# Performance work log

Measured on AMD Instinct MI355X. Metric: run time of the kernel, lower is better.

Reference implementation:

```python
import jax, jax.numpy as jnp
import numpy as np

N0, N1, N2 = 200000, 50000, 12500
E0, E1, E2 = 3200000, 800000, 200000
CIN, C, COUT = 4, 128, 1


def gcn(x, W, b, src, dst, n):
    # GCN conv with added self-loops and symmetric degree normalization
    h = x @ W
    loops = jnp.arange(n)
    s = jnp.concatenate([src, loops])
    d = jnp.concatenate([dst, loops])
    deg = jax.ops.segment_sum(jnp.ones(s.shape[0], h.dtype), d, num_segments=n)
    inv = jax.lax.rsqrt(jnp.maximum(deg, 1.0))
    msg = h[s] * (inv[s] * inv[d])[:, None]
    return jax.ops.segment_sum(msg, d, num_segments=n) + b


def pool_max(x, clusters, n_clusters):
    # cluster-based max pooling; empty clusters -> 0
    p = jax.ops.segment_max(x, clusters, num_segments=n_clusters)
    return jnp.where(jnp.isneginf(p), jnp.zeros_like(p), p)


def setup_inputs() -> dict:
    ks = jax.random.split(jax.random.key(0), 40)

    def w(k, i, o):
        return jax.random.normal(k, (i, o), jnp.float32) / np.float32(np.sqrt(i))

    inp = {
        'x': jax.random.normal(ks[0], (N0, CIN), jnp.float32),
        'edge_index0': jax.random.randint(ks[1], (2, E0), 0, N0),
        'edge_index1': jax.random.randint(ks[2], (2, E1), 0, N1),
        'edge_index2': jax.random.randint(ks[3], (2, E2), 0, N2),
        'clusters0': jax.random.randint(ks[4], (N0,), 0, N1),
        'clusters1': jax.random.randint(ks[5], (N1,), 0, N2),
        # encoder level 0
        'w_e0a': w(ks[6], CIN, C), 'b_e0a': jnp.zeros((C,), jnp.float32),
        'w_e0b': w(ks[7], C, C),   'b_e0b': jnp.zeros((C,), jnp.float32),
        # encoder level 1
        'w_e1a': w(ks[8], C, C),   'b_e1a': jnp.zeros((C,), jnp.float32),
        'w_e1b': w(ks[9], C, C),   'b_e1b': jnp.zeros((C,), jnp.float32),
        # bottom level 2
        'w_ba': w(ks[10], C, C),   'b_ba': jnp.zeros((C,), jnp.float32),
        'w_bb': w(ks[11], C, C),   'b_bb': jnp.zeros((C,), jnp.float32),
        # decoder level 1 (concat skip -> 2C in)
        'w_d1a': w(ks[12], 2 * C, C), 'b_d1a': jnp.zeros((C,), jnp.float32),
        'w_d1b': w(ks[13], C, C),     'b_d1b': jnp.zeros((C,), jnp.float32),
        # decoder level 0
        'w_d0a': w(ks[14], 2 * C, C), 'b_d0a': jnp.zeros((C,), jnp.float32),
        'w_d0b': w(ks[15], C, C),     'b_d0b': jnp.zeros((C,), jnp.float32),
        # output projection
        'w_out': w(ks[16], C, COUT), 'b_out': jnp.zeros((COUT,), jnp.float32),
    }
    return inp


def reference(x, edge_index0, edge_index1, edge_index2, clusters0, clusters1,
              w_e0a, b_e0a, w_e0b, b_e0b, w_e1a, b_e1a, w_e1b, b_e1b,
              w_ba, b_ba, w_bb, b_bb, w_d1a, b_d1a, w_d1b, b_d1b,
              w_d0a, b_d0a, w_d0b, b_d0b, w_out, b_out):
    n0 = x.shape[0]
    n1 = clusters1.shape[0]
    n2 = N2
    relu = jax.nn.relu
    s0, d0 = edge_index0[0], edge_index0[1]
    s1, d1 = edge_index1[0], edge_index1[1]
    s2, d2 = edge_index2[0], edge_index2[1]

    # encoder level 0
    e0 = relu(gcn(x, w_e0a, b_e0a, s0, d0, n0))
    e0 = relu(gcn(e0, w_e0b, b_e0b, s0, d0, n0))
    # pool -> level 1
    x1 = pool_max(e0, clusters0, n1)
    e1 = relu(gcn(x1, w_e1a, b_e1a, s1, d1, n1))
    e1 = relu(gcn(e1, w_e1b, b_e1b, s1, d1, n1))
    # pool -> level 2 (bottom)
    x2 = pool_max(e1, clusters1, n2)
    bt = relu(gcn(x2, w_ba, b_ba, s2, d2, n2))
    bt = relu(gcn(bt, w_bb, b_bb, s2, d2, n2))
    # unpool -> level 1, concat skip
    u1 = jnp.concatenate([bt[clusters1], e1], axis=1)
    dl1 = relu(gcn(u1, w_d1a, b_d1a, s1, d1, n1))
    dl1 = relu(gcn(dl1, w_d1b, b_d1b, s1, d1, n1))
    # unpool -> level 0, concat skip
    u0 = jnp.concatenate([dl1[clusters0], e0], axis=1)
    dl0 = relu(gcn(u0, w_d0a, b_d0a, s0, d0, n0))
    dl0 = relu(gcn(dl0, w_d0b, b_d0b, s0, d0, n0))
    # per-node output head
    return dl0 @ w_out + b_out
```

## Files before the change

kernel.cpp:

```cpp
#include <hip/hip_runtime.h>
#include <hip/hip_fp16.h>
#include <cstdint>
#include <cstddef>

#define PN0 200000
#define PN1 50000
#define PN2 12500
#define PE0 3200000
#define PE1 800000
#define PE2 200000

#define GCAP 64
#define CCAP 32

#define P0 0
#define P1 200192
#define P2 250368
#define P3 263168
#define P4 313344
#define CNT_END 326144
#define NBUCKETS 637
#define NITEMS 4450000
#define IPB 8192
#define NBLK 544

static inline int cdiv_i(int a, int b) { return (a + b - 1) / b; }

union H4 { uint4 q; uint2 u; __half2 h[2]; };

typedef _Float16 f16x8 __attribute__((ext_vector_type(8)));
typedef float f32x4 __attribute__((ext_vector_type(4)));
union F8 { uint4 q; f16x8 f; };

__device__ inline float2 load2f(const float* p) { return *(const float2*)p; }
__device__ inline float2 load2f(const __half* p) { return __half22float2(*(const __half2*)p); }


struct BSeg {
    const int* idx[5];
    const int* src[3];
    int item_off[5];
    int P[5];
    int colb[5];
    int cap[5];
    int nN[5];
    int ioff[3];
};

__device__ inline int seg_of_item(const BSeg& s, int i) {
    int seg = 0;
#pragma unroll
    for (int t = 1; t < 5; ++t) if (i >= s.item_off[t]) seg = t;
    return seg;
}
__device__ inline int seg_of_g(const BSeg& s, int g) {
    int seg = 0;
#pragma unroll
    for (int t = 1; t < 5; ++t) if (g >= s.P[t]) seg = t;
    return seg;
}

__global__ __launch_bounds__(256) void hist_k(BSeg s, int* __restrict__ BH) {
    __shared__ int lh[640];
    int tid = threadIdx.x;
    for (int k = tid; k < 640; k += 256) lh[k] = 0;
    __syncthreads();
    int base = blockIdx.x * IPB;
#pragma unroll 4
    for (int it = 0; it < 32; ++it) {
        int i = base + it * 256 + tid;
        if (i < NITEMS) {
            int seg = seg_of_item(s, i);
            int il = i - s.item_off[seg];
            int g = s.P[seg] + s.idx[seg][il];
            atomicAdd(&lh[g >> 9], 1);
        }
    }
    __syncthreads();
    for (int k = tid; k < 640; k += 256) BH[blockIdx.x * 640 + k] = lh[k];
}

__global__ __launch_bounds__(256) void scan_bh_k(int* __restrict__ BH, int* __restrict__ BT) {
    int b = blockIdx.x;
    int tid = threadIdx.x;
    __shared__ int tsum[256];
    int v[3];
    int base = tid * 3;
    int sum = 0;
#pragma unroll
    for (int k = 0; k < 3; ++k) {
        int idx = base + k;
        v[k] = (idx < NBLK) ? BH[idx * 640 + b] : 0;
        sum += v[k];
    }
    tsum[tid] = sum;
    __syncthreads();
    for (int off = 1; off < 256; off <<= 1) {
        int t = (tid >= off) ? tsum[tid - off] : 0;
        __syncthreads();
        tsum[tid] += t;
        __syncthreads();
    }
    int excl = tsum[tid] - sum;
#pragma unroll
    for (int k = 0; k < 3; ++k) {
        int idx = base + k;
        if (idx < NBLK) { BH[idx * 640 + b] = excl; excl += v[k]; }
    }
    if (tid == 255) BT[b] = tsum[255];
}

__global__ __launch_bounds__(1024) void bb_scan_k(const int* __restrict__ BT, int* __restrict__ BB) {
    __shared__ int sm[1024];
    int tid = threadIdx.x;
    int v = (tid < NBUCKETS) ? BT[tid] : 0;
    sm[tid] = v;
    __syncthreads();
    for (int off = 1; off < 1024; off <<= 1) {
        int t = (tid >= off) ? sm[tid - off] : 0;
        __syncthreads();
        sm[tid] += t;
        __syncthreads();
    }
    if (tid < NBUCKETS) BB[tid] = sm[tid] - v;
}

__global__ __launch_bounds__(256) void scatter_k(BSeg s, const int* __restrict__ BH,
                                                 const int* __restrict__ BB, int2* __restrict__ sorted) {
    __shared__ int lr[640];
    int tid = threadIdx.x;
    for (int k = tid; k < 640; k += 256) lr[k] = 0;
    __syncthreads();
    int base = blockIdx.x * IPB;
#pragma unroll 4
    for (int it = 0; it < 32; ++it) {
        int i = base + it * 256 + tid;
        if (i < NITEMS) {
            int seg = seg_of_item(s, i);
            int il = i - s.item_off[seg];
            int g = s.P[seg] + s.idx[seg][il];
            int val = (seg < 3) ? s.src[seg][il] : il;
            int b = g >> 9;
            int r = atomicAdd(&lr[b], 1);
            int pos = BB[b] + BH[blockIdx.x * 640 + b] + r;
            sorted[pos] = make_int2(g, val);
        }
    }
}

__global__ __launch_bounds__(256) void buildc_k(BSeg s, const int2* __restrict__ sorted,
                                                const int* __restrict__ BB, const int* __restrict__ BT,
                                                int* __restrict__ col, int* __restrict__ cnt,
                                                float* __restrict__ inv) {
    int b = blockIdx.x;
    int tid = threadIdx.x;
    __shared__ int lc[512];
    for (int k = tid; k < 512; k += 256) lc[k] = 0;
    __syncthreads();
    int start = BB[b], end = start + BT[b];
    for (int i = start + tid; i < end; i += 256) {
        int2 p = sorted[i];
        int g = p.x;
        int local = g & 511;
        int slot = atomicAdd(&lc[local], 1);
        int seg = seg_of_g(s, g);
        int d = g - s.P[seg];
        int cap = s.cap[seg];
        if (slot < cap) col[s.colb[seg] + d * cap + slot] = p.y;
    }
    __syncthreads();
    for (int local = tid; local < 512; local += 256) {
        int g = (b << 9) + local;
        int seg = seg_of_g(s, g);
        int d = g - s.P[seg];
        if (d < s.nN[seg]) {
            int c = lc[local];
            cnt[g] = c;
            if (seg < 3) inv[s.ioff[seg] + d] = rsqrtf((float)(c + 1));
        }
    }
}

struct PrepW { const float* src[11]; __half* dst[11]; };
__global__ __launch_bounds__(256) void prep_w_k(PrepW p) {
    const float* w = p.src[blockIdx.x];
    __half* o = p.dst[blockIdx.x];
    for (int i = threadIdx.x; i < 16384; i += 256) {
        int k = i >> 7, n = i & 127;
        o[n * 128 + k] = __float2half(w[i]);
    }
}


__global__ __launch_bounds__(256) void agg4_k(const float* __restrict__ X, float* __restrict__ O,
                                              const int* __restrict__ deg, const int* __restrict__ col,
                                              const float* __restrict__ inv, int N) {
    int v = blockIdx.x * 256 + threadIdx.x;
    if (v >= N) return;
    float iv = inv[v];
    float4 xv = *(const float4*)(X + (size_t)v * 4);
    float ax = xv.x * iv, ay = xv.y * iv, az = xv.z * iv, aw = xv.w * iv;
    int b0 = v * GCAP, b1 = b0 + deg[v];
    for (int j = b0; j < b1; ++j) {
        int u = col[j];
        float iu = inv[u];
        float4 xu = *(const float4*)(X + (size_t)u * 4);
        ax += xu.x * iu; ay += xu.y * iu; az += xu.z * iu; aw += xu.w * iu;
    }
    float4 o; o.x = ax * iv; o.y = ay * iv; o.z = az * iv; o.w = aw * iv;
    *(float4*)(O + (size_t)v * 4) = o;
}

__global__ __launch_bounds__(256) void gemm4_k(const float* __restrict__ XA, const float* __restrict__ W,
                                               const float* __restrict__ bias, __half* __restrict__ O, int N) {
    int wid = (blockIdx.x * 256 + threadIdx.x) >> 6;
    int lane = threadIdx.x & 63;
    if (wid >= N) return;
    float4 x = *(const float4*)(XA + (size_t)wid * 4);
    int c = lane * 2;
    float2 w0 = *(const float2*)(W + c);
    float2 w1 = *(const float2*)(W + 128 + c);
    float2 w2 = *(const float2*)(W + 256 + c);
    float2 w3 = *(const float2*)(W + 384 + c);
    float2 b = *(const float2*)(bias + c);
    float ox = b.x + x.x * w0.x + x.y * w1.x + x.z * w2.x + x.w * w3.x;
    float oy = b.y + x.x * w0.y + x.y * w1.y + x.z * w2.y + x.w * w3.y;
    ox = fmaxf(ox, 0.f); oy = fmaxf(oy, 0.f);
    *(__half2*)(O + (size_t)wid * 128 + c) = __floats2half2_rn(ox, oy);
}

__global__ __launch_bounds__(256) void agg_k(const __half* __restrict__ H, __half* __restrict__ O,
                                             const int* __restrict__ deg, const int* __restrict__ col,
                                             const float* __restrict__ inv, const float* __restrict__ bias,
                                             int N) {
    int wpair = (blockIdx.x * 256 + threadIdx.x) >> 6;
    int lane = threadIdx.x & 63;
    int v = wpair * 2 + (lane >> 5);
    int l32 = lane & 31;
    if (v >= N) return;
    float iv = inv[v];
    int c4 = l32 * 4;
    float4 a0 = {0,0,0,0}, a1 = {0,0,0,0}, a2 = {0,0,0,0}, a3 = {0,0,0,0};
    int b0 = v * GCAP, b1 = b0 + deg[v];
    int j = b0;
    for (; j + 8 <= b1; j += 8) {
        int u0 = col[j],     u1 = col[j + 1], u2 = col[j + 2], u3 = col[j + 3];
        int u4 = col[j + 4], u5 = col[j + 5], u6 = col[j + 6], u7 = col[j + 7];
        H4 t0, t1, t2, t3, t4, t5, t6, t7;
        t0.u = *(const uint2*)(H + (size_t)u0 * 128 + c4);
        t1.u = *(const uint2*)(H + (size_t)u1 * 128 + c4);
        t2.u = *(const uint2*)(H + (size_t)u2 * 128 + c4);
        t3.u = *(const uint2*)(H + (size_t)u3 * 128 + c4);
        t4.u = *(const uint2*)(H + (size_t)u4 * 128 + c4);
        t5.u = *(const uint2*)(H + (size_t)u5 * 128 + c4);
        t6.u = *(const uint2*)(H + (size_t)u6 * 128 + c4);
        t7.u = *(const uint2*)(H + (size_t)u7 * 128 + c4);
        float2 p, q;
        p = __half22float2(t0.h[0]); q = __half22float2(t0.h[1]);
        a0.x += p.x; a0.y += p.y; a0.z += q.x; a0.w += q.y;
        p = __half22float2(t1.h[0]); q = __half22float2(t1.h[1]);
        a1.x += p.x; a1.y += p.y; a1.z += q.x; a1.w += q.y;
        p = __half22float2(t2.h[0]); q = __half22float2(t2.h[1]);
        a2.x += p.x; a2.y += p.y; a2.z += q.x; a2.w += q.y;
        p = __half22float2(t3.h[0]); q = __half22float2(t3.h[1]);
        a3.x += p.x; a3.y += p.y; a3.z += q.x; a3.w += q.y;
        p = __half22float2(t4.h[0]); q = __half22float2(t4.h[1]);
        a0.x += p.x; a0.y += p.y; a0.z += q.x; a0.w += q.y;
        p = __half22float2(t5.h[0]); q = __half22float2(t5.h[1]);
        a1.x += p.x; a1.y += p.y; a1.z += q.x; a1.w += q.y;
        p = __half22float2(t6.h[0]); q = __half22float2(t6.h[1]);
        a2.x += p.x; a2.y += p.y; a2.z += q.x; a2.w += q.y;
        p = __half22float2(t7.h[0]); q = __half22float2(t7.h[1]);
        a3.x += p.x; a3.y += p.y; a3.z += q.x; a3.w += q.y;
    }
    for (; j + 4 <= b1; j += 4) {
        int u0 = col[j], u1 = col[j + 1], u2 = col[j + 2], u3 = col[j + 3];
        H4 t0, t1, t2, t3;
        t0.u = *(const uint2*)(H + (size_t)u0 * 128 + c4);
        t1.u = *(const uint2*)(H + (size_t)u1 * 128 + c4);
        t2.u = *(const uint2*)(H + (size_t)u2 * 128 + c4);
        t3.u = *(const uint2*)(H + (size_t)u3 * 128 + c4);
        float2 p, q;
        p = __half22float2(t0.h[0]); q = __half22float2(t0.h[1]);
        a0.x += p.x; a0.y += p.y; a0.z += q.x; a0.w += q.y;
        p = __half22float2(t1.h[0]); q = __half22float2(t1.h[1]);
        a1.x += p.x; a1.y += p.y; a1.z += q.x; a1.w += q.y;
        p = __half22float2(t2.h[0]); q = __half22float2(t2.h[1]);
        a2.x += p.x; a2.y += p.y; a2.z += q.x; a2.w += q.y;
        p = __half22float2(t3.h[0]); q = __half22float2(t3.h[1]);
        a3.x += p.x; a3.y += p.y; a3.z += q.x; a3.w += q.y;
    }
    for (; j < b1; ++j) {
        H4 t; t.u = *(const uint2*)(H + (size_t)col[j] * 128 + c4);
        float2 p = __half22float2(t.h[0]), q = __half22float2(t.h[1]);
        a0.x += p.x; a0.y += p.y; a0.z += q.x; a0.w += q.y;
    }
    {
        H4 t; t.u = *(const uint2*)(H + (size_t)v * 128 + c4);
        float2 p = __half22float2(t.h[0]), q = __half22float2(t.h[1]);
        a1.x += p.x; a1.y += p.y; a1.z += q.x; a1.w += q.y;
    }
    float4 s;
    s.x = (a0.x + a1.x) + (a2.x + a3.x);
    s.y = (a0.y + a1.y) + (a2.y + a3.y);
    s.z = (a0.z + a1.z) + (a2.z + a3.z);
    s.w = (a0.w + a1.w) + (a2.w + a3.w);
    float4 b = *(const float4*)(bias + c4);
    H4 t;
    t.h[0] = __floats2half2_rn(fmaxf(s.x * iv + b.x, 0.f), fmaxf(s.y * iv + b.y, 0.f));
    t.h[1] = __floats2half2_rn(fmaxf(s.z * iv + b.z, 0.f), fmaxf(s.w * iv + b.w, 0.f));
    *(uint2*)(O + (size_t)v * 128 + c4) = t.u;
}

__global__ __launch_bounds__(256) void agg_head_k(const __half* __restrict__ H,
                                                  const int* __restrict__ deg, const int* __restrict__ col,
                                                  const float* __restrict__ inv, const float* __restrict__ bias,
                                                  const float* __restrict__ wout, const float* __restrict__ bout,
                                                  float* __restrict__ out, int N) {
    int wpair = (blockIdx.x * 256 + threadIdx.x) >> 6;
    int lane = threadIdx.x & 63;
    int v = wpair * 2 + (lane >> 5);
    int l32 = lane & 31;
    if (v >= N) return;
    float iv = inv[v];
    int c4 = l32 * 4;
    float4 a0 = {0,0,0,0}, a1 = {0,0,0,0}, a2 = {0,0,0,0}, a3 = {0,0,0,0};
    int b0 = v * GCAP, b1 = b0 + deg[v];
    int j = b0;
    for (; j + 8 <= b1; j += 8) {
        int u0 = col[j],     u1 = col[j + 1], u2 = col[j + 2], u3 = col[j + 3];
        int u4 = col[j + 4], u5 = col[j + 5], u6 = col[j + 6], u7 = col[j + 7];
        H4 t0, t1, t2, t3, t4, t5, t6, t7;
        t0.u = *(const uint2*)(H + (size_t)u0 * 128 + c4);
        t1.u = *(const uint2*)(H + (size_t)u1 * 128 + c4);
        t2.u = *(const uint2*)(H + (size_t)u2 * 128 + c4);
        t3.u = *(const uint2*)(H + (size_t)u3 * 128 + c4);
        t4.u = *(const uint2*)(H + (size_t)u4 * 128 + c4);
        t5.u = *(const uint2*)(H + (size_t)u5 * 128 + c4);
        t6.u = *(const uint2*)(H + (size_t)u6 * 128 + c4);
        t7.u = *(const uint2*)(H + (size_t)u7 * 128 + c4);
        float2 p, q;
        p = __half22float2(t0.h[0]); q = __half22float2(t0.h[1]);
        a0.x += p.x; a0.y += p.y; a0.z += q.x; a0.w += q.y;
        p = __half22float2(t1.h[0]); q = __half22float2(t1.h[1]);
        a1.x += p.x; a1.y += p.y; a1.z += q.x; a1.w += q.y;
        p = __half22float2(t2.h[0]); q = __half22float2(t2.h[1]);
        a2.x += p.x; a2.y += p.y; a2.z += q.x; a2.w += q.y;
        p = __half22float2(t3.h[0]); q = __half22float2(t3.h[1]);
        a3.x += p.x; a3.y += p.y; a3.z += q.x; a3.w += q.y;
        p = __half22float2(t4.h[0]); q = __half22float2(t4.h[1]);
        a0.x += p.x; a0.y += p.y; a0.z += q.x; a0.w += q.y;
        p = __half22float2(t5.h[0]); q = __half22float2(t5.h[1]);
        a1.x += p.x; a1.y += p.y; a1.z += q.x; a1.w += q.y;
        p = __half22float2(t6.h[0]); q = __half22float2(t6.h[1]);
        a2.x += p.x; a2.y += p.y; a2.z += q.x; a2.w += q.y;
        p = __half22float2(t7.h[0]); q = __half22float2(t7.h[1]);
        a3.x += p.x; a3.y += p.y; a3.z += q.x; a3.w += q.y;
    }
    for (; j + 4 <= b1; j += 4) {
        int u0 = col[j], u1 = col[j + 1], u2 = col[j + 2], u3 = col[j + 3];
        H4 t0, t1, t2, t3;
        t0.u = *(const uint2*)(H + (size_t)u0 * 128 + c4);
        t1.u = *(const uint2*)(H + (size_t)u1 * 128 + c4);
        t2.u = *(const uint2*)(H + (size_t)u2 * 128 + c4);
        t3.u = *(const uint2*)(H + (size_t)u3 * 128 + c4);
        float2 p, q;
        p = __half22float2(t0.h[0]); q = __half22float2(t0.h[1]);
        a0.x += p.x; a0.y += p.y; a0.z += q.x; a0.w += q.y;
        p = __half22float2(t1.h[0]); q = __half22float2(t1.h[1]);
        a1.x += p.x; a1.y += p.y; a1.z += q.x; a1.w += q.y;
        p = __half22float2(t2.h[0]); q = __half22float2(t2.h[1]);
        a2.x += p.x; a2.y += p.y; a2.z += q.x; a2.w += q.y;
        p = __half22float2(t3.h[0]); q = __half22float2(t3.h[1]);
        a3.x += p.x; a3.y += p.y; a3.z += q.x; a3.w += q.y;
    }
    for (; j < b1; ++j) {
        H4 t; t.u = *(const uint2*)(H + (size_t)col[j] * 128 + c4);
        float2 p = __half22float2(t.h[0]), q = __half22float2(t.h[1]);
        a0.x += p.x; a0.y += p.y; a0.z += q.x; a0.w += q.y;
    }
    {
        H4 t; t.u = *(const uint2*)(H + (size_t)v * 128 + c4);
        float2 p = __half22float2(t.h[0]), q = __half22float2(t.h[1]);
        a1.x += p.x; a1.y += p.y; a1.z += q.x; a1.w += q.y;
    }
    float4 sm;
    sm.x = (a0.x + a1.x) + (a2.x + a3.x);
    sm.y = (a0.y + a1.y) + (a2.y + a3.y);
    sm.z = (a0.z + a1.z) + (a2.z + a3.z);
    sm.w = (a0.w + a1.w) + (a2.w + a3.w);
    float4 b = *(const float4*)(bias + c4);
    float4 w = *(const float4*)(wout + c4);
    float s = fmaxf(sm.x * iv + b.x, 0.f) * w.x
            + fmaxf(sm.y * iv + b.y, 0.f) * w.y
            + fmaxf(sm.z * iv + b.z, 0.f) * w.z
            + fmaxf(sm.w * iv + b.w, 0.f) * w.w;
    for (int off = 16; off >= 1; off >>= 1) s += __shfl_down(s, off, 32);
    if (l32 == 0) out[v] = s + bout[0];
}

__global__ __launch_bounds__(256) void pool_k(const __half* __restrict__ X, __half* __restrict__ O,
                                              const int* __restrict__ cdeg, const int* __restrict__ col,
                                              int Nc) {
    int wid = (blockIdx.x * 256 + threadIdx.x) >> 6;
    int lane = threadIdx.x & 63;
    if (wid >= Nc) return;
    int c = lane * 2;
    float mx = 0.f, my = 0.f;
    int b0 = wid * CCAP, b1 = b0 + cdeg[wid];
    for (int j = b0; j < b1; ++j) {
        int u = col[j];
        float2 t = load2f(X + (size_t)u * 128 + c);
        mx = fmaxf(mx, t.x); my = fmaxf(my, t.y);
    }
    *(__half2*)(O + (size_t)wid * 128 + c) = __floats2half2_rn(mx, my);
}

__global__ __launch_bounds__(256) void gemm_mfma_k(const __half* __restrict__ X, const __half* __restrict__ Wt,
                                                   __half* __restrict__ O, int N,
                                                   const int* __restrict__ cl, const __half* __restrict__ T,
                                                   const float* __restrict__ rowscale) {
    __shared__ __half Ws[128 * 136];
    int tid = threadIdx.x;
    for (int i = tid; i < 2048; i += 256) {
        int n = i >> 4, k = (i & 15) * 8;
        *(uint4*)(&Ws[n * 136 + k]) = *(const uint4*)(Wt + n * 128 + k);
    }
    __syncthreads();

    int wave = tid >> 6, lane = tid & 63;
    int quad = lane >> 4, m = lane & 15;
    int rowBase = blockIdx.x * 64 + wave * 16;
    int arow = rowBase + m;
    bool aok = arow < N;

    f16x8 afr[4];
    const __half* xrow = X + (size_t)arow * 128;
#pragma unroll
    for (int kc = 0; kc < 4; ++kc) {
        F8 t;
        if (aok) t.q = *(const uint4*)(xrow + kc * 32 + quad * 8);
        else { t.q.x = 0; t.q.y = 0; t.q.z = 0; t.q.w = 0; }
        afr[kc] = t.f;
    }

    f32x4 acc[8];
#pragma unroll
    for (int t = 0; t < 8; ++t) acc[t] = (f32x4){0.f, 0.f, 0.f, 0.f};

#pragma unroll
    for (int kc = 0; kc < 4; ++kc) {
#pragma unroll
        for (int t = 0; t < 8; ++t) {
            F8 b;
            b.q = *(const uint4*)(&Ws[(t * 16 + m) * 136 + kc * 32 + quad * 8]);
            acc[t] = __builtin_amdgcn_mfma_f32_16x16x32_f16(afr[kc], b.f, acc[t], 0, 0, 0);
        }
    }

    int baseRow = rowBase + quad * 4;
#pragma unroll
    for (int r = 0; r < 4; ++r) {
        int orow = baseRow + r;
        if (orow >= N) continue;
        float rs = rowscale ? rowscale[orow] : 1.0f;
        const __half* Trow = cl ? (T + (size_t)cl[orow] * 128) : nullptr;
#pragma unroll
        for (int t = 0; t < 8; ++t) {
            float v = acc[t][r];
            if (Trow) v += __half2float(Trow[t * 16 + m]);
            O[(size_t)orow * 128 + t * 16 + m] = __float2half(v * rs);
        }
    }
}


extern "C" void kernel_launch(void* const* d_in, const int* in_sizes, int n_in,
                              void* d_out, int out_size, void* d_ws, size_t ws_size,
                              hipStream_t stream) {
    const float* x        = (const float*)d_in[0];
    const int*   ei0      = (const int*)d_in[1];
    const int*   ei1      = (const int*)d_in[2];
    const int*   ei2      = (const int*)d_in[3];
    const int*   cl0      = (const int*)d_in[4];
    const int*   cl1      = (const int*)d_in[5];
    const float* w_e0a = (const float*)d_in[6];  const float* b_e0a = (const float*)d_in[7];
    const float* w_e0b = (const float*)d_in[8];  const float* b_e0b = (const float*)d_in[9];
    const float* w_e1a = (const float*)d_in[10]; const float* b_e1a = (const float*)d_in[11];
    const float* w_e1b = (const float*)d_in[12]; const float* b_e1b = (const float*)d_in[13];
    const float* w_ba  = (const float*)d_in[14]; const float* b_ba  = (const float*)d_in[15];
    const float* w_bb  = (const float*)d_in[16]; const float* b_bb  = (const float*)d_in[17];
    const float* w_d1a = (const float*)d_in[18]; const float* b_d1a = (const float*)d_in[19];
    const float* w_d1b = (const float*)d_in[20]; const float* b_d1b = (const float*)d_in[21];
    const float* w_d0a = (const float*)d_in[22]; const float* b_d0a = (const float*)d_in[23];
    const float* w_d0b = (const float*)d_in[24]; const float* b_d0b = (const float*)d_in[25];
    const float* w_out = (const float*)d_in[26]; const float* b_out = (const float*)d_in[27];
    float* out = (float*)d_out;

    const int N0 = PN0, N1 = PN1, N2 = PN2;
    const int E0 = PE0, E1 = PE1, E2 = PE2;

    char* base = (char*)d_ws;
    size_t off = 0;
    auto alloc = [&](size_t bytes) -> char* {
        char* p = base + off;
        off += (bytes + 255) & ~(size_t)255;
        return p;
    };
    __half* bufA  = (__half*)alloc((size_t)N0 * 128 * 2);
    __half* h0    = (__half*)alloc((size_t)N0 * 128 * 2);
    __half* h16   = (__half*)alloc((size_t)N1 * 128 * 2);
    __half* e1buf = (__half*)alloc((size_t)N1 * 128 * 2);
    __half* x1buf = (__half*)alloc((size_t)N1 * 128 * 2);
    __half* x2buf = (__half*)alloc((size_t)N2 * 128 * 2);
    __half* btbuf = (__half*)alloc((size_t)N2 * 128 * 2);
    __half* t2    = (__half*)alloc((size_t)N2 * 128 * 2);
    __half* t3    = (__half*)alloc((size_t)N1 * 128 * 2);
    float*  xa4   = (float*)alloc((size_t)N0 * 4 * 4);
    float*  INV   = (float*)alloc((size_t)(N0 + N1 + N2) * 4);
    int* CNT = (int*)alloc((size_t)CNT_END * 4);
    const int o0 = 0, o1 = N0 * GCAP, o2 = o1 + N1 * GCAP, o3 = o2 + N2 * GCAP, o4 = o3 + N1 * CCAP;
    const int colLen = o4 + N2 * CCAP;
    int* COL = (int*)alloc((size_t)colLen * 4);
    __half* WT = (__half*)alloc((size_t)11 * 128 * 128 * 2);
    int* BT = (int*)alloc(640 * 4);
    int* BB = (int*)alloc(640 * 4);
    if (off > ws_size) return;

    int2* sorted = (int2*)h0;
    int*  BH     = (int*)h16;

    float* inv0 = INV;
    float* inv1 = INV + N0;
    float* inv2 = INV + N0 + N1;
    int* deg0 = CNT + P0;  int* col0 = COL + o0;
    int* deg1 = CNT + P1;  int* col1 = COL + o1;
    int* deg2 = CNT + P2;  int* col2 = COL + o2;
    int* cdeg0 = CNT + P3; int* ccol0 = COL + o3;
    int* cdeg1 = CNT + P4; int* ccol1 = COL + o4;

    (void)n_in; (void)in_sizes; (void)out_size;

    BSeg bs;
    bs.idx[0] = ei0 + E0; bs.idx[1] = ei1 + E1; bs.idx[2] = ei2 + E2;
    bs.idx[3] = cl0;      bs.idx[4] = cl1;
    bs.src[0] = ei0; bs.src[1] = ei1; bs.src[2] = ei2;
    bs.item_off[0] = 0;            bs.item_off[1] = E0;                bs.item_off[2] = E0 + E1;
    bs.item_off[3] = E0 + E1 + E2; bs.item_off[4] = E0 + E1 + E2 + N0;
    bs.P[0] = P0; bs.P[1] = P1; bs.P[2] = P2; bs.P[3] = P3; bs.P[4] = P4;
    bs.colb[0] = o0; bs.colb[1] = o1; bs.colb[2] = o2; bs.colb[3] = o3; bs.colb[4] = o4;
    bs.cap[0] = GCAP; bs.cap[1] = GCAP; bs.cap[2] = GCAP; bs.cap[3] = CCAP; bs.cap[4] = CCAP;
    bs.nN[0] = N0; bs.nN[1] = N1; bs.nN[2] = N2; bs.nN[3] = N1; bs.nN[4] = N2;
    bs.ioff[0] = 0; bs.ioff[1] = N0; bs.ioff[2] = N0 + N1;

    hist_k<<<NBLK, 256, 0, stream>>>(bs, BH);
    scan_bh_k<<<NBUCKETS, 256, 0, stream>>>(BH, BT);
    bb_scan_k<<<1, 1024, 0, stream>>>(BT, BB);
    scatter_k<<<NBLK, 256, 0, stream>>>(bs, BH, BB, sorted);
    buildc_k<<<NBUCKETS, 256, 0, stream>>>(bs, sorted, BB, BT, COL, CNT, INV);

    __half* wt_e0b = WT;                __half* wt_e1a = WT + 16384;
    __half* wt_e1b = WT + 2 * 16384;    __half* wt_ba  = WT + 3 * 16384;
    __half* wt_bb  = WT + 4 * 16384;    __half* wt_d1aT = WT + 5 * 16384;
    __half* wt_d1aB = WT + 6 * 16384;   __half* wt_d1b = WT + 7 * 16384;
    __half* wt_d0aT = WT + 8 * 16384;   __half* wt_d0aB = WT + 9 * 16384;
    __half* wt_d0b = WT + 10 * 16384;
    PrepW pw;
    pw.src[0] = w_e0b;  pw.dst[0] = wt_e0b;
    pw.src[1] = w_e1a;  pw.dst[1] = wt_e1a;
    pw.src[2] = w_e1b;  pw.dst[2] = wt_e1b;
    pw.src[3] = w_ba;   pw.dst[3] = wt_ba;
    pw.src[4] = w_bb;   pw.dst[4] = wt_bb;
    pw.src[5] = w_d1a;            pw.dst[5] = wt_d1aT;
    pw.src[6] = w_d1a + 16384;    pw.dst[6] = wt_d1aB;
    pw.src[7] = w_d1b;  pw.dst[7] = wt_d1b;
    pw.src[8] = w_d0a;            pw.dst[8] = wt_d0aT;
    pw.src[9] = w_d0a + 16384;    pw.dst[9] = wt_d0aB;
    pw.src[10] = w_d0b; pw.dst[10] = wt_d0b;
    prep_w_k<<<11, 256, 0, stream>>>(pw);

    auto mfma = [&](const __half* X, const __half* Wt, __half* O, int N,
                    const int* cl, const __half* T, const float* rs) {
        gemm_mfma_k<<<cdiv_i(N, 64), 256, 0, stream>>>(X, Wt, O, N, cl, T, rs);
    };
    auto agg = [&](const __half* H, __half* O, const int* deg, const int* col, const float* inv,
                   const float* bias, int N) {
        agg_k<<<cdiv_i(N, 8), 256, 0, stream>>>(H, O, deg, col, inv, bias, N);
    };

    agg4_k<<<cdiv_i(N0, 256), 256, 0, stream>>>(x, xa4, deg0, col0, inv0, N0);
    gemm4_k<<<cdiv_i(N0, 4), 256, 0, stream>>>(xa4, w_e0a, b_e0a, bufA, N0);
    mfma(bufA, wt_e0b, h0, N0, nullptr, nullptr, inv0);
    agg(h0, bufA, deg0, col0, inv0, b_e0b, N0);
    pool_k<<<cdiv_i(N1, 4), 256, 0, stream>>>(bufA, x1buf, cdeg0, ccol0, N1);
    mfma(x1buf, wt_e1a, h16, N1, nullptr, nullptr, inv1);
    agg(h16, e1buf, deg1, col1, inv1, b_e1a, N1);
    mfma(e1buf, wt_e1b, h16, N1, nullptr, nullptr, inv1);
    agg(h16, e1buf, deg1, col1, inv1, b_e1b, N1);
    pool_k<<<cdiv_i(N2, 4), 256, 0, stream>>>(e1buf, x2buf, cdeg1, ccol1, N2);
    mfma(x2buf, wt_ba, h16, N2, nullptr, nullptr, inv2);
    agg(h16, btbuf, deg2, col2, inv2, b_ba, N2);
    mfma(btbuf, wt_bb, h16, N2, nullptr, nullptr, inv2);
    agg(h16, btbuf, deg2, col2, inv2, b_bb, N2);
    mfma(btbuf, wt_d1aT, t2, N2, nullptr, nullptr, nullptr);
    mfma(e1buf, wt_d1aB, h16, N1, cl1, t2, inv1);
    agg(h16, x1buf, deg1, col1, inv1, b_d1a, N1);
    mfma(x1buf, wt_d1b, h16, N1, nullptr, nullptr, inv1);
    agg(h16, x1buf, deg1, col1, inv1, b_d1b, N1);
    mfma(x1buf, wt_d0aT, t3, N1, nullptr, nullptr, nullptr);
    mfma(bufA, wt_d0aB, h0, N0, cl0, t3, inv0);
    agg(h0, bufA, deg0, col0, inv0, b_d0a, N0);
    mfma(bufA, wt_d0b, h0, N0, nullptr, nullptr, inv0);
    agg_head_k<<<cdiv_i(N0, 8), 256, 0, stream>>>(h0, deg0, col0, inv0, b_d0b,
                                                  w_out, b_out, out, N0);
}
```

Measured before the change: 1.190 ms.

## Reorder aggregation nodes by degree to balance wavefront work

Adds a per-level counting sort of nodes by in-degree (histogram, scan, scatter kernels) that produces a permutation array. The aggregation kernels then process nodes in that order, so the half-wavefronts paired together have similar degrees and lose less time to divergent loop trip counts. The cost is three extra setup kernels, an extra indirection per node, and scattered output writes in place of sequential ones.

```diff
diff --git a/kernel.cpp b/kernel.cpp
--- a/kernel.cpp
+++ b/kernel.cpp
@@ -23,6 +23,11 @@
 #define NITEMS 4450000
 #define IPB 8192
 #define NBLK 544
+
+#define DB0 196
+#define DB1 49
+#define DB2 13
+#define DBLK 258
 
 static inline int cdiv_i(int a, int b) { return (a + b - 1) / b; }
 
@@ -181,6 +186,74 @@
     }
 }
 
+
+__device__ inline void dlevel(int b, int& base, int& N, int& cntOff, int& permBase) {
+    if (b < DB0)            { base = b * 1024;               N = PN0; cntOff = P0; permBase = 0; }
+    else if (b < DB0 + DB1) { base = (b - DB0) * 1024;       N = PN1; cntOff = P1; permBase = PN0; }
+    else                    { base = (b - DB0 - DB1) * 1024; N = PN2; cntOff = P2; permBase = PN0 + PN1; }
+}
+
+__global__ __launch_bounds__(256) void dhist_k(const int* __restrict__ CNT, int* __restrict__ DH) {
+    __shared__ int lh[65];
+    int tid = threadIdx.x;
+    if (tid < 65) lh[tid] = 0;
+    __syncthreads();
+    int base, N, cntOff, permBase;
+    dlevel(blockIdx.x, base, N, cntOff, permBase);
+#pragma unroll
+    for (int k = 0; k < 4; ++k) {
+        int i = base + k * 256 + tid;
+        if (i < N) atomicAdd(&lh[min(CNT[cntOff + i], 64)], 1);
+    }
+    __syncthreads();
+    if (tid < 65) DH[blockIdx.x * 65 + tid] = lh[tid];
+}
+
+__global__ __launch_bounds__(256) void dscan_k(int* __restrict__ DH) {
+    int p = threadIdx.x;
+    __shared__ int tot[195];
+    if (p < 195) {
+        int L = p / 65, bin = p % 65;
+        int Bs = (L == 0) ? 0 : (L == 1 ? DB0 : DB0 + DB1);
+        int Be = (L == 0) ? DB0 : (L == 1 ? DB0 + DB1 : DBLK);
+        int run = 0;
+        for (int b = Bs; b < Be; ++b) { int v = DH[b * 65 + bin]; DH[b * 65 + bin] = run; run += v; }
+        tot[p] = run;
+    }
+    __syncthreads();
+    if (p < 3) {
+        int run = 0;
+        for (int bin = 0; bin < 65; ++bin) { int v = tot[p * 65 + bin]; tot[p * 65 + bin] = run; run += v; }
+    }
+    __syncthreads();
+    if (p < 195) {
+        int L = p / 65, bin = p % 65;
+        int Bs = (L == 0) ? 0 : (L == 1 ? DB0 : DB0 + DB1);
+        int Be = (L == 0) ? DB0 : (L == 1 ? DB0 + DB1 : DBLK);
+        int basev = tot[p];
+        for (int b = Bs; b < Be; ++b) DH[b * 65 + bin] += basev;
+    }
+}
+
+__global__ __launch_bounds__(256) void dscatter_k(const int* __restrict__ CNT, const int* __restrict__ DH,
+                                                  int* __restrict__ PERM) {
+    __shared__ int lc[65];
+    int tid = threadIdx.x;
+    if (tid < 65) lc[tid] = 0;
+    __syncthreads();
+    int base, N, cntOff, permBase;
+    dlevel(blockIdx.x, base, N, cntOff, permBase);
+#pragma unroll
+    for (int k = 0; k < 4; ++k) {
+        int i = base + k * 256 + tid;
+        if (i < N) {
+            int d = min(CNT[cntOff + i], 64);
+            int r = atomicAdd(&lc[d], 1);
+            PERM[permBase + DH[blockIdx.x * 65 + d] + r] = i;
+        }
+    }
+}
+
 struct PrepW { const float* src[11]; __half* dst[11]; };
 __global__ __launch_bounds__(256) void prep_w_k(PrepW p) {
     const float* w = p.src[blockIdx.x];
@@ -194,9 +267,11 @@
 
 __global__ __launch_bounds__(256) void agg4_k(const float* __restrict__ X, float* __restrict__ O,
                                               const int* __restrict__ deg, const int* __restrict__ col,
-                                              const float* __restrict__ inv, int N) {
-    int v = blockIdx.x * 256 + threadIdx.x;
-    if (v >= N) return;
+                                              const float* __restrict__ inv, const int* __restrict__ perm,
+                                              int N) {
+    int i = blockIdx.x * 256 + threadIdx.x;
+    if (i >= N) return;
+    int v = perm[i];
     float iv = inv[v];
     float4 xv = *(const float4*)(X + (size_t)v * 4);
     float ax = xv.x * iv, ay = xv.y * iv, az = xv.z * iv, aw = xv.w * iv;
@@ -232,12 +307,13 @@
 __global__ __launch_bounds__(256) void agg_k(const __half* __restrict__ H, __half* __restrict__ O,
                                              const int* __restrict__ deg, const int* __restrict__ col,
                                              const float* __restrict__ inv, const float* __restrict__ bias,
-                                             int N) {
+                                             const int* __restrict__ perm, int N) {
     int wpair = (blockIdx.x * 256 + threadIdx.x) >> 6;
     int lane = threadIdx.x & 63;
-    int v = wpair * 2 + (lane >> 5);
+    int idx = wpair * 2 + (lane >> 5);
     int l32 = lane & 31;
-    if (v >= N) return;
+    if (idx >= N) return;
+    int v = perm[idx];
     float iv = inv[v];
     int c4 = l32 * 4;
     float4 a0 = {0,0,0,0}, a1 = {0,0,0,0}, a2 = {0,0,0,0}, a3 = {0,0,0,0};
@@ -316,12 +392,14 @@
                                                   const int* __restrict__ deg, const int* __restrict__ col,
                                                   const float* __restrict__ inv, const float* __restrict__ bias,
                                                   const float* __restrict__ wout, const float* __restrict__ bout,
+                                                  const int* __restrict__ perm,
                                                   float* __restrict__ out, int N) {
     int wpair = (blockIdx.x * 256 + threadIdx.x) >> 6;
     int lane = threadIdx.x & 63;
-    int v = wpair * 2 + (lane >> 5);
+    int idx = wpair * 2 + (lane >> 5);
     int l32 = lane & 31;
-    if (v >= N) return;
+    if (idx >= N) return;
+    int v = perm[idx];
     float iv = inv[v];
     int c4 = l32 * 4;
     float4 a0 = {0,0,0,0}, a1 = {0,0,0,0}, a2 = {0,0,0,0}, a3 = {0,0,0,0};
@@ -525,6 +603,8 @@
     __half* WT = (__half*)alloc((size_t)11 * 128 * 128 * 2);
     int* BT = (int*)alloc(640 * 4);
     int* BB = (int*)alloc(640 * 4);
+    int* DH = (int*)alloc((size_t)DBLK * 65 * 4);
+    int* PERM = (int*)alloc((size_t)(N0 + N1 + N2) * 4);
     if (off > ws_size) return;
 
     int2* sorted = (int2*)h0;
@@ -538,6 +618,9 @@
     int* deg2 = CNT + P2;  int* col2 = COL + o2;
     int* cdeg0 = CNT + P3; int* ccol0 = COL + o3;
     int* cdeg1 = CNT + P4; int* ccol1 = COL + o4;
+    int* perm0 = PERM;
+    int* perm1 = PERM + N0;
+    int* perm2 = PERM + N0 + N1;
 
     (void)n_in; (void)in_sizes; (void)out_size;
 
@@ -558,6 +641,10 @@
     bb_scan_k<<<1, 1024, 0, stream>>>(BT, BB);
     scatter_k<<<NBLK, 256, 0, stream>>>(bs, BH, BB, sorted);
     buildc_k<<<NBUCKETS, 256, 0, stream>>>(bs, sorted, BB, BT, COL, CNT, INV);
+
+    dhist_k<<<DBLK, 256, 0, stream>>>(CNT, DH);
+    dscan_k<<<1, 256, 0, stream>>>(DH);
+    dscatter_k<<<DBLK, 256, 0, stream>>>(CNT, DH, PERM);
 
     __half* wt_e0b = WT;                __half* wt_e1a = WT + 16384;
     __half* wt_e1b = WT + 2 * 16384;    __half* wt_ba  = WT + 3 * 16384;
@@ -584,33 +671,33 @@
         gemm_mfma_k<<<cdiv_i(N, 64), 256, 0, stream>>>(X, Wt, O, N, cl, T, rs);
     };
     auto agg = [&](const __half* H, __half* O, const int* deg, const int* col, const float* inv,
-                   const float* bias, int N) {
-        agg_k<<<cdiv_i(N, 8), 256, 0, stream>>>(H, O, deg, col, inv, bias, N);
+                   const float* bias, const int* perm, int N) {
+        agg_k<<<cdiv_i(N, 8), 256, 0, stream>>>(H, O, deg, col, inv, bias, perm, N);
     };
 
-    agg4_k<<<cdiv_i(N0, 256), 256, 0, stream>>>(x, xa4, deg0, col0, inv0, N0);
+    agg4_k<<<cdiv_i(N0, 256), 256, 0, stream>>>(x, xa4, deg0, col0, inv0, perm0, N0);
     gemm4_k<<<cdiv_i(N0, 4), 256, 0, stream>>>(xa4, w_e0a, b_e0a, bufA, N0);
     mfma(bufA, wt_e0b, h0, N0, nullptr, nullptr, inv0);
-    agg(h0, bufA, deg0, col0, inv0, b_e0b, N0);
+    agg(h0, bufA, deg0, col0, inv0, b_e0b, perm0, N0);
     pool_k<<<cdiv_i(N1, 4), 256, 0, stream>>>(bufA, x1buf, cdeg0, ccol0, N1);
     mfma(x1buf, wt_e1a, h16, N1, nullptr, nullptr, inv1);
-    agg(h16, e1buf, deg1, col1, inv1, b_e1a, N1);
+    agg(h16, e1buf, deg1, col1, inv1, b_e1a, perm1, N1);
     mfma(e1buf, wt_e1b, h16, N1, nullptr, nullptr, inv1);
-    agg(h16, e1buf, deg1, col1, inv1, b_e1b, N1);
+    agg(h16, e1buf, deg1, col1, inv1, b_e1b, perm1, N1);
     pool_k<<<cdiv_i(N2, 4), 256, 0, stream>>>(e1buf, x2buf, cdeg1, ccol1, N2);
     mfma(x2buf, wt_ba, h16, N2, nullptr, nullptr, inv2);
-    agg(h16, btbuf, deg2, col2, inv2, b_ba, N2);
+    agg(h16, btbuf, deg2, col2, inv2, b_ba, perm2, N2);
     mfma(btbuf, wt_bb, h16, N2, nullptr, nullptr, inv2);
-    agg(h16, btbuf, deg2, col2, inv2, b_bb, N2);
+    agg(h16, btbuf, deg2, col2, inv2, b_bb, perm2, N2);
     mfma(btbuf, wt_d1aT, t2, N2, nullptr, nullptr, nullptr);
     mfma(e1buf, wt_d1aB, h16, N1, cl1, t2, inv1);
-    agg(h16, x1buf, deg1, col1, inv1, b_d1a, N1);
+    agg(h16, x1buf, deg1, col1, inv1, b_d1a, perm1, N1);
     mfma(x1buf, wt_d1b, h16, N1, nullptr, nullptr, inv1);
-    agg(h16, x1buf, deg1, col1, inv1, b_d1b, N1);
+    agg(h16, x1buf, deg1, col1, inv1, b_d1b, perm1, N1);
     mfma(x1buf, wt_d0aT, t3, N1, nullptr, nullptr, nullptr);
     mfma(bufA, wt_d0aB, h0, N0, cl0, t3, inv0);
-    agg(h0, bufA, deg0, col0, inv0, b_d0a, N0);
+    agg(h0, bufA, deg0, col0, inv0, b_d0a, perm0, N0);
     mfma(bufA, wt_d0b, h0, N0, nullptr, nullptr, inv0);
     agg_head_k<<<cdiv_i(N0, 8), 256, 0, stream>>>(h0, deg0, col0, inv0, b_d0b,
-                                                  w_out, b_out, out, N0);
-}
+                                                  w_out, b_out, perm0, out, N0);
+}
```

Result: slower. 1.261 ms (+5.9%).
